# Optimization experiments

Measured on AMD Instinct MI355X. Metric: run time of the kernel, lower is better.

The kernel has to match this reference:

```python
import jax, jax.numpy as jnp
import numpy as np

B, T, F, H, K = 512, 128, 256, 512, 3

def setup_inputs() -> dict:
    key = jax.random.key(0)
    ks = jax.random.split(key, 8)
    x = jax.random.normal(ks[0], (B, T, F), dtype=jnp.float32)
    theta = jnp.ones((F,), dtype=jnp.float32)                 # selector logits
    Wx = jax.random.normal(ks[1], (F, H), dtype=jnp.float32) * 0.1
    Wh = jax.random.normal(ks[2], (H, H), dtype=jnp.float32) * 0.1
    b = jnp.zeros((H,), dtype=jnp.float32)
    c = jax.random.normal(ks[3], (H, K), dtype=jnp.float32)   # fuzzy centers
    sigma = jnp.ones((H, K), dtype=jnp.float32)               # fuzzy widths
    q = jax.random.normal(ks[4], (H, K), dtype=jnp.float32)   # rule consequents
    Wc = jax.random.normal(ks[5], (H, 1), dtype=jnp.float32) * 0.05  # classifier
    bc = jnp.zeros((1,), dtype=jnp.float32)
    return dict(x=x, theta=theta, Wx=Wx, Wh=Wh, b=b, c=c, sigma=sigma, q=q, Wc=Wc, bc=bc)


def reference(x, theta, Wx, Wh, b, c, sigma, q, Wc, bc):
    weights = jax.nn.sigmoid(theta)                 # [F]
    xf = x * weights                                # [B,T,F]
    # x_t @ Wx is used twice per step (for z_t and new_info); precompute once for all t.
    xw = jnp.einsum('btf,fh->bth', xf, Wx)          # [B,T,H]
    new_info = jnp.tanh(xw)                         # [B,T,H]
    inv_den = 1.0 / (2.0 * sigma ** 2 + 1e-8)       # [H,K]

    def step(h, inp):
        xw_t, new_t = inp                           # [B,H], [B,H]
        z = xw_t + h @ Wh + b                       # [B,H]
        mu = jnp.exp(-(z[..., None] - c) ** 2 * inv_den)   # [B,H,K]
        g = jax.nn.sigmoid(jnp.sum(mu * q, axis=-1) / (jnp.sum(mu, axis=-1) + 1e-8))
        h = (1.0 - g) * h + g * new_t
        return h, None

    h0 = jnp.zeros((x.shape[0], Wh.shape[0]), dtype=x.dtype)
    h, _ = jax.lax.scan(step, h0, (jnp.swapaxes(xw, 0, 1), jnp.swapaxes(new_info, 0, 1)))
    logits = h @ Wc + bc                            # [B,1]
    return logits, weights
```

## Files before the change

### kernel.cpp

```cpp
#include <hip/hip_runtime.h>
#include <hip/hip_bf16.h>


#define B_  512
#define T_  128
#define F_  256
#define H_  512
#define LOG2E 1.4426950408889634f

#define XW_T_STRIDE 262144

typedef __attribute__((ext_vector_type(8))) short short8;
typedef __attribute__((ext_vector_type(4))) float float4v;
typedef __attribute__((ext_vector_type(4))) int int4i;

__device__ inline ushort f2bf(float f) {
  __hip_bfloat16 h = __float2bfloat16(f);
  return *reinterpret_cast<ushort*>(&h);
}
__device__ inline float bf2f(unsigned u) { return __uint_as_float(u << 16); }
__device__ inline float fexp2(float x) { return __builtin_amdgcn_exp2f(x); }
__device__ inline float frcp(float x) { return __builtin_amdgcn_rcpf(x); }

#define WS_W2I8 67108864
#define WS_WXF  67371008
#define WS_GP8  67633152
#define WS_BVEC 67649536
#define WS_WCV  67651584
#define WS_SCOL 67653632
#define WS_WTS  67657728

__global__ void prep_small(const float* __restrict__ theta,
                           const float* __restrict__ b,
                           const float* __restrict__ c,
                           const float* __restrict__ sigma,
                           const float* __restrict__ q,
                           const float* __restrict__ Wc,
                           float* __restrict__ out_w,
                           float* __restrict__ gp8,
                           float* __restrict__ bvec,
                           float* __restrict__ wcv,
                           float* __restrict__ wts) {
  const int i = threadIdx.x;
  if (i < F_) {
    float w = 1.f / (1.f + __expf(-theta[i]));
    out_w[i] = w;
    wts[i] = w;
  }
  {
    float a[3], cc[3], qq[3];
#pragma unroll
    for (int k = 0; k < 3; ++k) {
      float s = sigma[i * 3 + k];
      cc[k] = c[i * 3 + k];
      a[k] = -LOG2E / (2.f * s * s + 1e-8f);
      qq[k] = q[i * 3 + k];
    }
    gp8[i * 8 + 0] = cc[0];
    gp8[i * 8 + 1] = cc[1];
    gp8[i * 8 + 2] = cc[2];
    gp8[i * 8 + 3] = a[0];
    gp8[i * 8 + 4] = a[1];
    gp8[i * 8 + 5] = a[2];
    gp8[i * 8 + 6] = __uint_as_float((unsigned)f2bf(qq[0]) |
                                     ((unsigned)f2bf(qq[1]) << 16));
    gp8[i * 8 + 7] = __uint_as_float((unsigned)f2bf(qq[2]));
    bvec[i] = b[i];
    wcv[i] = Wc[i];
  }
}

__global__ __launch_bounds__(256) void prep_weights(
    const float* __restrict__ Wh, const float* __restrict__ Wx,
    int* __restrict__ W2, ushort* __restrict__ WxF,
    float* __restrict__ scol) {
  __shared__ float lds[16544];
  const int t = threadIdx.x;

  if (blockIdx.x < 32) {
    const int nb = blockIdx.x;
    const int cc = t & 15, rg = t >> 4;
    float m = 0.f;
#pragma unroll
    for (int s = 0; s < 32; ++s)
      m = fmaxf(m, fabsf(Wh[(rg + s * 16) * H_ + nb * 16 + cc]));
    lds[rg * 16 + cc] = m;
    __syncthreads();
    if (t < 16) {
      float mm = lds[t];
#pragma unroll
      for (int s = 1; s < 16; ++s) mm = fmaxf(mm, lds[s * 16 + t]);
      mm = fmaxf(mm, 1e-20f);
      scol[nb * 16 + t] = mm / (127.f * 127.f);
      lds[256 + t] = 127.f / mm;
    }
    __syncthreads();
    const int lane = t & 63, dw = t >> 6;
    const int n = nb * 16 + (lane & 15);
    const float iv = lds[256 + (lane & 15)];
#pragma unroll
    for (int kt = 0; kt < 8; ++kt) {
      int pk = 0;
#pragma unroll
      for (int jj = 0; jj < 4; ++jj) {
        const int k = kt * 64 + ((lane >> 4) << 4) + dw * 4 + jj;
        int qv = (int)rintf(Wh[k * H_ + n] * iv);
        qv = min(127, max(-127, qv));
        pk |= (qv & 255) << (8 * jj);
      }
      W2[((kt * 32 + nb) * 64 + lane) * 4 + dw] = pk;
    }
  } else {
    const int kt = blockIdx.x - 32;
#pragma unroll
    for (int it = 0; it < 16; ++it) {
      const int lin = (it * 256 + t) * 4;
      const float4 v = *(const float4*)(Wx + kt * 32 * H_ + lin);
      const int f = lin >> 9, n0 = lin & 511;
      lds[f * 517 + n0 + 0] = v.x;
      lds[f * 517 + n0 + 1] = v.y;
      lds[f * 517 + n0 + 2] = v.z;
      lds[f * 517 + n0 + 3] = v.w;
    }
    __syncthreads();
#pragma unroll
    for (int it = 0; it < 8; ++it) {
      const int o = (it * 256 + t) * 8;
      const int lane = (o >> 3) & 63, nb = o >> 9;
      const int n = nb * 16 + (lane & 15), fb = (lane >> 4) << 3;
      ushort v[8];
#pragma unroll
      for (int j = 0; j < 8; ++j) v[j] = f2bf(lds[(fb + j) * 517 + n]);
      *(short8*)(WxF + kt * 16384 + o) = *(short8*)v;
    }
  }
}

__global__ __launch_bounds__(256, 1) void gemm1_kernel(
    const float* __restrict__ x, const float* __restrict__ wts,
    const ushort* __restrict__ WxF, ushort* __restrict__ xw2) {
  __shared__ ushort A[64 * 264];
  const int tid = threadIdx.x;
  const int lane = tid & 63, wg = tid >> 6;
  const int col16 = lane & 15, quad = lane >> 4;
  const int tt = blockIdx.x, bb = blockIdx.y;

  {
    const float4 wv = *(const float4*)(wts + lane * 4);
#pragma unroll
    for (int it = 0; it < 16; ++it) {
      const int row = it * 4 + wg;
      float4 xv = *(const float4*)(x + ((size_t)(bb * 64 + row) * T_ + tt) * F_ + lane * 4);
      ushort4 o;
      o.x = f2bf(xv.x * wv.x);
      o.y = f2bf(xv.y * wv.y);
      o.z = f2bf(xv.z * wv.z);
      o.w = f2bf(xv.w * wv.w);
      *(ushort4*)&A[row * 264 + lane * 4] = o;
    }
  }
  __syncthreads();

  const float4v zero = {0.f, 0.f, 0.f, 0.f};
#pragma unroll
  for (int nn = 0; nn < 2; ++nn) {
    float4v acc[16];
#pragma unroll
    for (int i = 0; i < 16; ++i) acc[i] = zero;
#pragma unroll
    for (int kt = 0; kt < 8; ++kt) {
      short8 af = *(const short8*)&A[(wg * 16 + col16) * 264 + kt * 32 + quad * 8];
      short8 bfv[16];
#pragma unroll
      for (int nt = 0; nt < 16; ++nt)
        bfv[nt] = *(const short8*)(WxF + ((kt * 32 + nn * 16 + nt) * 64 + lane) * 8);
#pragma unroll
      for (int nt = 0; nt < 16; ++nt)
        acc[nt] = __builtin_amdgcn_mfma_f32_16x16x32_bf16(af, bfv[nt], acc[nt], 0, 0, 0);
    }
#pragma unroll
    for (int nt = 0; nt < 16; ++nt) {
      ushort2 lo, hi;
      lo.x = f2bf(acc[nt][0]);
      lo.y = f2bf(acc[nt][1]);
      hi.x = f2bf(acc[nt][2]);
      hi.y = f2bf(acc[nt][3]);
      const int bg0 = bb * 32 + wg * 8 + quad * 2;
      const size_t off0 =
          (((size_t)tt * 256 + bg0) * 8 + nn * 4 + (nt >> 2)) * 128 +
          ((nt & 3) * 16 + col16) * 2;
      *(ushort2*)(xw2 + off0) = lo;
      *(ushort2*)(xw2 + off0 + 1024) = hi;
    }
  }
}

__global__ __launch_bounds__(512, 2) void scan4_kernel(
    const ushort* __restrict__ xw2, const int4i* __restrict__ W2,
    const float* __restrict__ gp8, const float* __restrict__ bvec,
    const float* __restrict__ wcv, const float* __restrict__ scol,
    const float* __restrict__ bc, float* __restrict__ out) {
  __shared__ char hb[2][1152];
  __shared__ float red[8][2];
  const int tid = threadIdx.x;
  const int lane = tid & 63, w = tid >> 6;
  const int col16 = lane & 15, quad = lane >> 4;
  const int bg = blockIdx.x;

  for (int i = tid; i < 576; i += 512) ((int*)hb)[i] = 0;

  int4i bfr[8][4];
#pragma unroll
  for (int kt = 0; kt < 8; ++kt)
#pragma unroll
    for (int nt = 0; nt < 4; ++nt)
      bfr[kt][nt] = W2[(kt * 32 + w * 4 + nt) * 64 + lane];

  const int col = w * 64 + lane;
  const float bcol = bvec[col], scl = scol[col], wcl = wcv[col];
  float4v g0 = *(const float4v*)(gp8 + col * 8);
  float4v g1 = *(const float4v*)(gp8 + col * 8 + 4);
  const float c0v = g0[0], c1v = g0[1], c2v = g0[2];
  const float a0v = g0[3], a1v = g1[0], a2v = g1[1];
  unsigned p01 = __float_as_uint(g1[2]);
  const float q0v = bf2f(p01 & 0xffffu);
  const float q1v = bf2f(p01 >> 16);
  const float q2v = bf2f(__float_as_uint(g1[3]) & 0xffffu);

  const unsigned wsel = (lane & 1) ? 0x0501u : 0x0004u;
  const int woff = col + ((lane & 1) ? 575 : 0);

  float hreg[2] = {0.f, 0.f};
  const int4i izero = {0, 0, 0, 0};
  int4i areg[8];
#pragma unroll
  for (int kt = 0; kt < 8; ++kt) areg[kt] = izero;

  const ushort* xwb = xw2 + ((size_t)bg * 8 + w) * 128 + lane * 2;
  unsigned xv = *(const unsigned*)xwb;
  unsigned xn;
  __syncthreads();

#pragma clang loop unroll(disable)
  for (int t = 0; t < T_; ++t) {
    const int tn = (t + 1) & 127;
    xn = *(const unsigned*)(xwb + (size_t)tn * XW_T_STRIDE);

    if (col16 < 2) {
      const char* abase = hb[t & 1] + col16 * 576;
#pragma unroll
      for (int kt = 0; kt < 8; ++kt)
        areg[kt] = *(const int4i*)(abase + kt * 64 + (quad << 4));
    }

    int4i acc[4];
#pragma unroll
    for (int nt = 0; nt < 4; ++nt) acc[nt] = izero;
#pragma unroll
    for (int kt = 0; kt < 8; ++kt)
#pragma unroll
      for (int nt = 0; nt < 4; ++nt)
        acc[nt] = __builtin_amdgcn_mfma_i32_16x16x64_i8(areg[kt], bfr[kt][nt], acc[nt], 0, 0, 0);

    int accq[2];
#pragma unroll
    for (int rg = 0; rg < 2; ++rg) {
      int t0 = __shfl(acc[0][rg], col16, 64);
      int t1 = __shfl(acc[1][rg], col16, 64);
      int t2 = __shfl(acc[2][rg], col16, 64);
      int t3 = __shfl(acc[3][rg], col16, 64);
      int sA = (quad & 1) ? t1 : t0;
      int sB = (quad & 1) ? t3 : t2;
      accq[rg] = (quad & 2) ? sB : sA;
    }

    int qb[2];
#pragma unroll
    for (int rg = 0; rg < 2; ++rg) {
      float v = __uint_as_float(rg ? (xv & 0xffff0000u) : (xv << 16));
      float z = v + bcol + (float)accq[rg] * scl;
      float e = fexp2(v * (2.f * LOG2E));
      float nw = 1.f - 2.f * frcp(1.f + e);
      float d0 = z - c0v, d1 = z - c1v, d2 = z - c2v;
      float m0 = fexp2(d0 * d0 * a0v);
      float m1 = fexp2(d1 * d1 * a1v);
      float m2 = fexp2(d2 * d2 * a2v);
      float num = m0 * q0v + m1 * q1v + m2 * q2v;
      float den = m0 + m1 + m2 + 1e-8f;
      float s = num * frcp(den);
      float gg = frcp(1.f + fexp2(-s * LOG2E));
      float h = hreg[rg] + gg * (nw - hreg[rg]);
      hreg[rg] = h;
      qb[rg] = (int)rintf(h * 127.f);
    }

    if (t < T_ - 1) {
      int pk = (qb[0] & 255) | ((qb[1] & 255) << 8);
      unsigned p1 = (unsigned)__shfl_xor(pk, 1, 64);
      unsigned v16 = __builtin_amdgcn_perm((unsigned)pk, p1, wsel);
      *(ushort*)(hb[(t + 1) & 1] + woff) = (ushort)v16;
      __syncthreads();
    }
    xv = xn;
  }

  float part[2];
#pragma unroll
  for (int rg = 0; rg < 2; ++rg) {
    part[rg] = hreg[rg] * wcl;
#pragma unroll
    for (int m = 1; m < 64; m <<= 1) part[rg] += __shfl_xor(part[rg], m, 64);
  }
  if (lane == 0) {
    red[w][0] = part[0];
    red[w][1] = part[1];
  }
  __syncthreads();
  if (tid < 2) {
    float s = bc[0];
#pragma unroll
    for (int ww = 0; ww < 8; ++ww) s += red[ww][tid];
    out[bg * 2 + tid] = s;
  }
}

extern "C" void kernel_launch(void* const* d_in, const int* in_sizes, int n_in,
                              void* d_out, int out_size, void* d_ws, size_t ws_size,
                              hipStream_t stream) {
  const float* x     = (const float*)d_in[0];
  const float* theta = (const float*)d_in[1];
  const float* Wx    = (const float*)d_in[2];
  const float* Wh    = (const float*)d_in[3];
  const float* b     = (const float*)d_in[4];
  const float* c     = (const float*)d_in[5];
  const float* sigma = (const float*)d_in[6];
  const float* q     = (const float*)d_in[7];
  const float* Wc    = (const float*)d_in[8];
  const float* bc    = (const float*)d_in[9];
  float* out = (float*)d_out;

  ushort* xw2 = (ushort*)d_ws;
  int*    W2  = (int*)((char*)d_ws + WS_W2I8);
  ushort* WxF = (ushort*)((char*)d_ws + WS_WXF);
  float*  gp8 = (float*)((char*)d_ws + WS_GP8);
  float*  bv  = (float*)((char*)d_ws + WS_BVEC);
  float*  wcv = (float*)((char*)d_ws + WS_WCV);
  float*  scl = (float*)((char*)d_ws + WS_SCOL);
  float*  wts = (float*)((char*)d_ws + WS_WTS);

  hipLaunchKernelGGL(prep_small, dim3(1), dim3(512), 0, stream,
                     theta, b, c, sigma, q, Wc, out + B_, gp8, bv, wcv, wts);
  hipLaunchKernelGGL(prep_weights, dim3(40), dim3(256), 0, stream,
                     Wh, Wx, W2, WxF, scl);
  hipLaunchKernelGGL(gemm1_kernel, dim3(128, 8), dim3(256), 0, stream,
                     x, wts, WxF, xw2);
  hipLaunchKernelGGL(scan4_kernel, dim3(256), dim3(512), 0, stream,
                     xw2, (const int4i*)W2, gp8, bv, wcv, scl, bc, out);
}
```

Baseline: 272.0 us.

## Fuse prep kernels, split MFMA chain for early shuffles, expand gaussian exponent algebraically

```diff
diff --git a/kernel.cpp b/kernel.cpp
--- a/kernel.cpp
+++ b/kernel.cpp
@@ -30,50 +30,15 @@
 #define WS_SCOL 67653632
 #define WS_WTS  67657728
 
-__global__ void prep_small(const float* __restrict__ theta,
-                           const float* __restrict__ b,
-                           const float* __restrict__ c,
-                           const float* __restrict__ sigma,
-                           const float* __restrict__ q,
-                           const float* __restrict__ Wc,
-                           float* __restrict__ out_w,
-                           float* __restrict__ gp8,
-                           float* __restrict__ bvec,
-                           float* __restrict__ wcv,
-                           float* __restrict__ wts) {
-  const int i = threadIdx.x;
-  if (i < F_) {
-    float w = 1.f / (1.f + __expf(-theta[i]));
-    out_w[i] = w;
-    wts[i] = w;
-  }
-  {
-    float a[3], cc[3], qq[3];
-#pragma unroll
-    for (int k = 0; k < 3; ++k) {
-      float s = sigma[i * 3 + k];
-      cc[k] = c[i * 3 + k];
-      a[k] = -LOG2E / (2.f * s * s + 1e-8f);
-      qq[k] = q[i * 3 + k];
-    }
-    gp8[i * 8 + 0] = cc[0];
-    gp8[i * 8 + 1] = cc[1];
-    gp8[i * 8 + 2] = cc[2];
-    gp8[i * 8 + 3] = a[0];
-    gp8[i * 8 + 4] = a[1];
-    gp8[i * 8 + 5] = a[2];
-    gp8[i * 8 + 6] = __uint_as_float((unsigned)f2bf(qq[0]) |
-                                     ((unsigned)f2bf(qq[1]) << 16));
-    gp8[i * 8 + 7] = __uint_as_float((unsigned)f2bf(qq[2]));
-    bvec[i] = b[i];
-    wcv[i] = Wc[i];
-  }
-}
-
 __global__ __launch_bounds__(256) void prep_weights(
     const float* __restrict__ Wh, const float* __restrict__ Wx,
+    const float* __restrict__ theta, const float* __restrict__ b,
+    const float* __restrict__ c, const float* __restrict__ sigma,
+    const float* __restrict__ q, const float* __restrict__ Wc,
     int* __restrict__ W2, ushort* __restrict__ WxF,
-    float* __restrict__ scol) {
+    float* __restrict__ scol, float* __restrict__ out_w,
+    float* __restrict__ gp8, float* __restrict__ bvec,
+    float* __restrict__ wcv, float* __restrict__ wts) {
   __shared__ float lds[16544];
   const int t = threadIdx.x;
 
@@ -110,7 +75,7 @@
       }
       W2[((kt * 32 + nb) * 64 + lane) * 4 + dw] = pk;
     }
-  } else {
+  } else if (blockIdx.x < 40) {
     const int kt = blockIdx.x - 32;
 #pragma unroll
     for (int it = 0; it < 16; ++it) {
@@ -132,6 +97,35 @@
 #pragma unroll
       for (int j = 0; j < 8; ++j) v[j] = f2bf(lds[(fb + j) * 517 + n]);
       *(short8*)(WxF + kt * 16384 + o) = *(short8*)v;
+    }
+  } else {
+#pragma unroll
+    for (int r = 0; r < 2; ++r) {
+      const int i = t + r * 256;
+      if (i < F_) {
+        float w = 1.f / (1.f + __expf(-theta[i]));
+        out_w[i] = w;
+        wts[i] = w;
+      }
+      float a[3], cc[3], qq[3];
+#pragma unroll
+      for (int k = 0; k < 3; ++k) {
+        float s = sigma[i * 3 + k];
+        cc[k] = c[i * 3 + k];
+        a[k] = -LOG2E / (2.f * s * s + 1e-8f);
+        qq[k] = q[i * 3 + k];
+      }
+      gp8[i * 8 + 0] = cc[0];
+      gp8[i * 8 + 1] = cc[1];
+      gp8[i * 8 + 2] = cc[2];
+      gp8[i * 8 + 3] = a[0];
+      gp8[i * 8 + 4] = a[1];
+      gp8[i * 8 + 5] = a[2];
+      gp8[i * 8 + 6] = __uint_as_float((unsigned)f2bf(qq[0]) |
+                                       ((unsigned)f2bf(qq[1]) << 16));
+      gp8[i * 8 + 7] = __uint_as_float((unsigned)f2bf(qq[2]));
+      bvec[i] = b[i];
+      wcv[i] = Wc[i];
     }
   }
 }
@@ -200,7 +194,7 @@
     const float* __restrict__ gp8, const float* __restrict__ bvec,
     const float* __restrict__ wcv, const float* __restrict__ scol,
     const float* __restrict__ bc, float* __restrict__ out) {
-  __shared__ char hb[2][1152];
+  __shared__ __align__(16) char hb[2][1152];
   __shared__ float red[8][2];
   const int tid = threadIdx.x;
   const int lane = tid & 63, w = tid >> 6;
@@ -226,6 +220,9 @@
   const float q0v = bf2f(p01 & 0xffffu);
   const float q1v = bf2f(p01 >> 16);
   const float q2v = bf2f(__float_as_uint(g1[3]) & 0xffffu);
+  const float b0v = -2.f * a0v * c0v, d0v = a0v * c0v * c0v;
+  const float b1v = -2.f * a1v * c1v, d1v = a1v * c1v * c1v;
+  const float b2v = -2.f * a2v * c2v, d2v = a2v * c2v * c2v;
 
   const unsigned wsel = (lane & 1) ? 0x0501u : 0x0004u;
   const int woff = col + ((lane & 1) ? 575 : 0);
@@ -253,24 +250,36 @@
         areg[kt] = *(const int4i*)(abase + kt * 64 + (quad << 4));
     }
 
-    int4i acc[4];
-#pragma unroll
-    for (int nt = 0; nt < 4; ++nt) acc[nt] = izero;
-#pragma unroll
-    for (int kt = 0; kt < 8; ++kt)
-#pragma unroll
-      for (int nt = 0; nt < 4; ++nt)
-        acc[nt] = __builtin_amdgcn_mfma_i32_16x16x64_i8(areg[kt], bfr[kt][nt], acc[nt], 0, 0, 0);
+    int4i acc0 = izero, acc1 = izero;
+#pragma unroll
+    for (int kt = 0; kt < 8; ++kt) {
+      acc0 = __builtin_amdgcn_mfma_i32_16x16x64_i8(areg[kt], bfr[kt][0], acc0, 0, 0, 0);
+      acc1 = __builtin_amdgcn_mfma_i32_16x16x64_i8(areg[kt], bfr[kt][1], acc1, 0, 0, 0);
+    }
+    int t0[2], t1[2];
+#pragma unroll
+    for (int rg = 0; rg < 2; ++rg) {
+      t0[rg] = __shfl(acc0[rg], col16, 64);
+      t1[rg] = __shfl(acc1[rg], col16, 64);
+    }
+    int4i acc2 = izero, acc3 = izero;
+#pragma unroll
+    for (int kt = 0; kt < 8; ++kt) {
+      acc2 = __builtin_amdgcn_mfma_i32_16x16x64_i8(areg[kt], bfr[kt][2], acc2, 0, 0, 0);
+      acc3 = __builtin_amdgcn_mfma_i32_16x16x64_i8(areg[kt], bfr[kt][3], acc3, 0, 0, 0);
+    }
+    int t2[2], t3[2];
+#pragma unroll
+    for (int rg = 0; rg < 2; ++rg) {
+      t2[rg] = __shfl(acc2[rg], col16, 64);
+      t3[rg] = __shfl(acc3[rg], col16, 64);
+    }
 
     int accq[2];
 #pragma unroll
     for (int rg = 0; rg < 2; ++rg) {
-      int t0 = __shfl(acc[0][rg], col16, 64);
-      int t1 = __shfl(acc[1][rg], col16, 64);
-      int t2 = __shfl(acc[2][rg], col16, 64);
-      int t3 = __shfl(acc[3][rg], col16, 64);
-      int sA = (quad & 1) ? t1 : t0;
-      int sB = (quad & 1) ? t3 : t2;
+      int sA = (quad & 1) ? t1[rg] : t0[rg];
+      int sB = (quad & 1) ? t3[rg] : t2[rg];
       accq[rg] = (quad & 2) ? sB : sA;
     }
 
@@ -281,10 +290,10 @@
       float z = v + bcol + (float)accq[rg] * scl;
       float e = fexp2(v * (2.f * LOG2E));
       float nw = 1.f - 2.f * frcp(1.f + e);
-      float d0 = z - c0v, d1 = z - c1v, d2 = z - c2v;
-      float m0 = fexp2(d0 * d0 * a0v);
-      float m1 = fexp2(d1 * d1 * a1v);
-      float m2 = fexp2(d2 * d2 * a2v);
+      float zz = z * z;
+      float m0 = fexp2(fmaf(a0v, zz, fmaf(b0v, z, d0v)));
+      float m1 = fexp2(fmaf(a1v, zz, fmaf(b1v, z, d1v)));
+      float m2 = fexp2(fmaf(a2v, zz, fmaf(b2v, z, d2v)));
       float num = m0 * q0v + m1 * q1v + m2 * q2v;
       float den = m0 + m1 + m2 + 1e-8f;
       float s = num * frcp(den);
@@ -295,7 +304,7 @@
     }
 
     if (t < T_ - 1) {
-      int pk = (qb[0] & 255) | ((qb[1] & 255) << 8);
+      int pk = (int)__builtin_amdgcn_perm((unsigned)qb[1], (unsigned)qb[0], 0x0400u);
       unsigned p1 = (unsigned)__shfl_xor(pk, 1, 64);
       unsigned v16 = __builtin_amdgcn_perm((unsigned)pk, p1, wsel);
       *(ushort*)(hb[(t + 1) & 1] + woff) = (ushort)v16;
@@ -348,10 +357,9 @@
   float*  scl = (float*)((char*)d_ws + WS_SCOL);
   float*  wts = (float*)((char*)d_ws + WS_WTS);
 
-  hipLaunchKernelGGL(prep_small, dim3(1), dim3(512), 0, stream,
-                     theta, b, c, sigma, q, Wc, out + B_, gp8, bv, wcv, wts);
-  hipLaunchKernelGGL(prep_weights, dim3(40), dim3(256), 0, stream,
-                     Wh, Wx, W2, WxF, scl);
+  hipLaunchKernelGGL(prep_weights, dim3(41), dim3(256), 0, stream,
+                     Wh, Wx, theta, b, c, sigma, q, Wc,
+                     W2, WxF, scl, out + B_, gp8, bv, wcv, wts);
   hipLaunchKernelGGL(gemm1_kernel, dim3(128, 8), dim3(256), 0, stream,
                      x, wts, WxF, xw2);
   hipLaunchKernelGGL(scan4_kernel, dim3(256), dim3(512), 0, stream,
```

New measurement: 266.3 us. 1.02x faster.
